# Performance work log

Hardware: AMD Instinct MI355X
Metric: run time of the kernel (lower is better)

The kernel has to match this reference:

```python
import jax, jax.numpy as jnp
import numpy as np
import math

B, S, P, G = 8, 512, 64, 64
E, GE = 768, 32          # sub_embed_dim, gene_embed_dim
HD = E // 2              # sub_head_dim = 384
L = P * G
LAMBDA_INIT = 0.8 - 0.6 * math.exp(-0.3 * 0)  # depth=0 -> 0.2
SCALING = HD ** -0.5


def setup_inputs() -> dict:
    key0 = jax.random.key(0)
    ks = jax.random.split(key0, 12)
    init = 0.02
    return {
        "query": jax.random.normal(ks[0], (B, S, E), jnp.float32),
        "key": jax.random.normal(ks[1], (B, P, G, GE), jnp.float32),
        "query_mask": jax.random.bernoulli(ks[2], 0.9, (B, S)),
        "key_mask": jax.random.bernoulli(ks[3], 0.9, (B, P, G)),
        # weights stored [in, out] so y = x @ W (equiv to torch Linear no-bias)
        "Wq": jax.random.normal(ks[4], (E, E), jnp.float32) * init,
        "Wkv": jax.random.normal(ks[5], (GE, 2 * E), jnp.float32) * init,
        "Wout": jax.random.normal(ks[6], (E, E), jnp.float32) * init,
        "lambda_q1": jax.random.normal(ks[7], (HD,), jnp.float32) * 0.1,
        "lambda_k1": jax.random.normal(ks[8], (HD,), jnp.float32) * 0.1,
        "lambda_q2": jax.random.normal(ks[9], (HD,), jnp.float32) * 0.1,
        "lambda_k2": jax.random.normal(ks[10], (HD,), jnp.float32) * 0.1,
        "ln_weight": jnp.ones((E,), jnp.float32),  # RMSNorm affine weight (2*HD = E)
    }


def reference(query, key, query_mask, key_mask, Wq, Wkv, Wout,
              lambda_q1, lambda_k1, lambda_q2, lambda_k2, ln_weight):
    # Projections
    Q = query @ Wq                                   # [B,S,E]
    KV = key.reshape(B, L, GE) @ Wkv                 # [B,L,2E]
    K = KV[..., :E]                                  # [B,L,E]
    V = KV[..., E:]                                  # [B,L,E] (= 2*HD)

    # Split into 2 heads of dim HD
    Qh = Q.reshape(B, S, 2, HD).transpose(0, 2, 1, 3) * SCALING   # [B,2,S,HD]
    Kh = K.reshape(B, L, 2, HD).transpose(0, 2, 1, 3)             # [B,2,L,HD]

    # Combined mask [B,S,L]
    mask = query_mask[:, :, None] & key_mask.reshape(B, L)[:, None, :]

    # Dual attention scores + stable softmax (eps=1e-8 on denominator)
    scores = jnp.einsum('bhsd,bhld->bhsl', Qh, Kh)                # [B,2,S,L]
    scores = jnp.where(mask[:, None], scores, -1e20)
    m = jnp.max(scores, axis=-1, keepdims=True)
    p = jnp.exp(scores - m)
    attn = p / (jnp.sum(p, axis=-1, keepdims=True) + 1e-8)

    # Differential combination
    lam = (jnp.exp(jnp.sum(lambda_q1 * lambda_k1))
           - jnp.exp(jnp.sum(lambda_q2 * lambda_k2)) + LAMBDA_INIT)
    diff = attn[:, 0] - lam * attn[:, 1]                          # [B,S,L]
    diff = diff - jnp.min(diff, axis=-1, keepdims=True) + 1e-20
    diff = jnp.where(mask, diff, 0.0)

    # Value contraction: [B,S,L] @ [B,L,E] -> [B,S,E]
    attn_out = jnp.einsum('bsl,ble->bse', diff, V)

    # RMSNorm (eps=1e-5, affine) then scale by (1 - lambda_init)
    ms = jnp.mean(attn_out * attn_out, axis=-1, keepdims=True)
    attn_out = attn_out * jax.lax.rsqrt(ms + 1e-5) * ln_weight
    attn_out = attn_out * (1.0 - LAMBDA_INIT)

    out = attn_out @ Wout                                         # [B,S,E]
    return out, diff.reshape(B, S, P, G)
```

## Files before the change

kernel.cpp:

```cpp
#include <hip/hip_runtime.h>
#include <math.h>

#define LAM_INIT 0.2f
#define ONE_MINUS_LAM 0.8f
#define SCALING_F 0.05103103630798288f

typedef _Float16 h2 __attribute__((ext_vector_type(2)));

#if defined(__has_builtin)
#if __has_builtin(__builtin_amdgcn_fdot2)
#define FDOT2(a, b, c) __builtin_amdgcn_fdot2((a), (b), (c), false)
#endif
#endif
#ifndef FDOT2
#define FDOT2(a, b, c) ((float)(a).x * (float)(b).x + ((float)(a).y * (float)(b).y + (c)))
#endif

__device__ inline float waveMin(float v) {
#pragma unroll
    for (int o = 32; o > 0; o >>= 1) v = fminf(v, __shfl_xor(v, o));
    return v;
}
__device__ inline float waveSum(float v) {
#pragma unroll
    for (int o = 32; o > 0; o >>= 1) v += __shfl_xor(v, o);
    return v;
}

__global__ __launch_bounds__(256) void k01_prep(
    const float* __restrict__ key, const float* __restrict__ Wq,
    const float* __restrict__ Wkv, const float* __restrict__ Wout,
    const float* __restrict__ lq1, const float* __restrict__ lk1,
    const float* __restrict__ lq2, const float* __restrict__ lk2,
    const float* __restrict__ ln,
    unsigned* __restrict__ keyThU, float* __restrict__ Wcp,
    float* __restrict__ Wvp, float* __restrict__ lam,
    float* __restrict__ M)
{
    int blk = blockIdx.x;
    int tid = threadIdx.x;
    if (blk < 128) {
        int b  = blk >> 4;
        int l0 = (blk & 15) << 8;
        __shared__ float tile[256 * 33];
        const float* kp = key + ((size_t)b * 4096 + l0) * 32;
#pragma unroll
        for (int q = 0; q < 32; ++q) {
            int idx = tid + (q << 8);
            int r = idx >> 5, g = idx & 31;
            tile[r * 33 + g] = kp[idx];
        }
        __syncthreads();
#pragma unroll
        for (int gp = 0; gp < 16; ++gp) {
            h2 v;
            v.x = (_Float16)tile[tid * 33 + 2 * gp];
            v.y = (_Float16)tile[tid * 33 + 2 * gp + 1];
            keyThU[((size_t)(b * 16 + gp)) * 4096 + l0 + tid] =
                __builtin_bit_cast(unsigned, v);
        }
    } else if (blk < 512) {
        int bb = blk - 128;
        int kc = bb & 1;
        int ob = bb >> 1;
        int idx = ob * 256 + tid;
        int e  = idx >> 6;
        int hg = idx & 63;
        int h = hg >> 5, g = hg & 31;
        const float4* wqr = (const float4*)(Wq  + (size_t)e * 768 + h * 384 + kc * 192);
        const float4* wkr = (const float4*)(Wkv + (size_t)g * 1536 + h * 384 + kc * 192);
        float s0 = 0.f, s1 = 0.f;
#pragma unroll 4
        for (int d = 0; d < 48; d += 2) {
            float4 a0 = wqr[d],   b0 = wkr[d];
            float4 a1 = wqr[d+1], b1 = wkr[d+1];
            s0 += a0.x*b0.x + a0.y*b0.y + a0.z*b0.z + a0.w*b0.w;
            s1 += a1.x*b1.x + a1.y*b1.y + a1.z*b1.z + a1.w*b1.w;
        }
        Wcp[kc * 49152 + idx] = (s0 + s1) * SCALING_F;
    } else if (blk < 1280) {
        int bb = blk - 512;
        int kc = bb / 96;
        int ob = bb - kc * 96;
        int idx = ob * 256 + tid;
        int g = idx / 768;
        int e = idx - g * 768;
        const float* wvr = Wkv + (size_t)g * 1536 + 768;
        int c0 = kc * 96;
        float s0 = 0.f, s1 = 0.f;
#pragma unroll 4
        for (int c = c0; c < c0 + 96; c += 2) {
            s0 += wvr[c]   * ln[c]   * Wout[(size_t)c * 768 + e];
            s1 += wvr[c+1] * ln[c+1] * Wout[(size_t)(c+1) * 768 + e];
        }
        Wvp[kc * 24576 + idx] = s0 + s1;
    } else if (blk == 1280) {
        float s1 = 0.f, s2 = 0.f;
        for (int d = tid; d < 384; d += 256) {
            s1 += lq1[d] * lk1[d];
            s2 += lq2[d] * lk2[d];
        }
        s1 = waveSum(s1);
        s2 = waveSum(s2);
        __shared__ float r1[4], r2[4];
        int wid = tid >> 6, lane = tid & 63;
        if (lane == 0) { r1[wid] = s1; r2[wid] = s2; }
        __syncthreads();
        if (tid == 0) {
            float a  = r1[0] + r1[1] + r1[2] + r1[3];
            float b2 = r2[0] + r2[1] + r2[2] + r2[3];
            lam[0] = expf(a) - expf(b2) + LAM_INIT;
        }
    } else {
        int idx = (blk - 1281) * 256 + tid;
        int g = idx >> 5, gp = idx & 31;
        const float4* ra = (const float4*)(Wkv + (size_t)g  * 1536 + 768);
        const float4* rb = (const float4*)(Wkv + (size_t)gp * 1536 + 768);
        float s = 0.f;
#pragma unroll 4
        for (int q = 0; q < 192; ++q) {
            float4 a = ra[q], b = rb[q];
            s += a.x*b.x + a.y*b.y + a.z*b.z + a.w*b.w;
        }
        M[idx] = s;
    }
}

__global__ __launch_bounds__(256) void k2_qt(
    const float* __restrict__ query, const float* __restrict__ Wcp,
    const float* __restrict__ Wvp, float* __restrict__ WvoT,
    float* __restrict__ Qtp)
{
    int blk = blockIdx.x;
    int tid = threadIdx.x;
    if (blk >= 512) {
        int idx = (blk - 512) * 256 + tid;
        float s = 0.f;
#pragma unroll
        for (int kc = 0; kc < 8; ++kc) s += Wvp[kc * 24576 + idx];
        int g = idx / 768;
        int e = idx - g * 768;
        WvoT[(size_t)e * 32 + g] = s;
        return;
    }
    int kc = blk >> 7;
    int mt = blk & 127;
    int m0 = mt * 32;
    __shared__ __align__(16) float As[64 * 33];
    __shared__ __align__(16) float Bs[64 * 64];

    int tm = tid >> 5;
    int tn = tid & 31;
    float acc[4][2];
#pragma unroll
    for (int r = 0; r < 4; ++r) { acc[r][0] = 0.f; acc[r][1] = 0.f; }

    for (int ch = 0; ch < 3; ++ch) {
        int k0 = kc * 192 + ch * 64;
        __syncthreads();
#pragma unroll
        for (int q = 0; q < 2; ++q) {
            int f = tid + q * 256;
            int m = f >> 4, kq = f & 15;
            float4 v = *(const float4*)&query[(size_t)(m0 + m) * 768 + k0 + kq * 4];
            As[(kq * 4 + 0) * 33 + m] = v.x;
            As[(kq * 4 + 1) * 33 + m] = v.y;
            As[(kq * 4 + 2) * 33 + m] = v.z;
            As[(kq * 4 + 3) * 33 + m] = v.w;
        }
#pragma unroll
        for (int q = 0; q < 4; ++q) {
            int f = tid + q * 256;
            int kk = f >> 4, n4 = f & 15;
            float4 a = *(const float4*)&Wcp[(size_t)(k0 + kk) * 64 + n4 * 4];
            float4 b = *(const float4*)&Wcp[49152 + (size_t)(k0 + kk) * 64 + n4 * 4];
            float4 s; s.x = a.x + b.x; s.y = a.y + b.y; s.z = a.z + b.z; s.w = a.w + b.w;
            *(float4*)&Bs[kk * 64 + n4 * 4] = s;
        }
        __syncthreads();
#pragma unroll 8
        for (int kk = 0; kk < 64; ++kk) {
            float4 a = *(const float4*)&As[kk * 33 + tm * 4];
            float2 b = *(const float2*)&Bs[kk * 64 + tn * 2];
            acc[0][0] += a.x * b.x; acc[0][1] += a.x * b.y;
            acc[1][0] += a.y * b.x; acc[1][1] += a.y * b.y;
            acc[2][0] += a.z * b.x; acc[2][1] += a.z * b.y;
            acc[3][0] += a.w * b.x; acc[3][1] += a.w * b.y;
        }
    }
#pragma unroll
    for (int r = 0; r < 4; ++r) {
        float2 o; o.x = acc[r][0]; o.y = acc[r][1];
        *(float2*)&Qtp[(size_t)kc * 262144 + (size_t)(m0 + tm * 4 + r) * 64 + tn * 2] = o;
    }
}

__global__ __launch_bounds__(512, 4) void k3_attn(
    const float* __restrict__ Qtp, const unsigned* __restrict__ keyThU,
    const int* __restrict__ qmask, const int* __restrict__ kmask,
    const float* __restrict__ lamp, float* __restrict__ diffO)
{
    int blk = blockIdx.x;
    int b  = blk >> 7;
    int s0 = (blk & 127) * 4;
    int tid = threadIdx.x;
    int lane = tid & 63, wid = tid >> 6;

    __shared__ __align__(16) unsigned qt_th[128];
    __shared__ float redS[64];
    __shared__ float redM[32];

    if (tid < 128) {
        int ts = tid >> 5;
        int h  = (tid >> 4) & 1;
        int gp = tid & 15;
        size_t row = (size_t)(b * 512 + s0 + ts) * 64;
        int col = h * 32 + 2 * gp;
        float v0 = 0.f, v1 = 0.f;
#pragma unroll
        for (int kc = 0; kc < 4; ++kc) {
            v0 += Qtp[(size_t)kc * 262144 + row + col];
            v1 += Qtp[(size_t)kc * 262144 + row + col + 1];
        }
        h2 hv; hv.x = (_Float16)v0; hv.y = (_Float16)v1;
        qt_th[gp * 8 + ts * 2 + h] = __builtin_bit_cast(unsigned, hv);
    }
    int qm[4];
#pragma unroll
    for (int ts = 0; ts < 4; ++ts) qm[ts] = qmask[b * 512 + s0 + ts];
    float lam = lamp[0];

    unsigned kmb = 0;
#pragma unroll
    for (int c = 0; c < 2; ++c) {
        int4 km = *(const int4*)(kmask + b * 4096 + c * 2048 + tid * 4);
        if (km.x) kmb |= 1u << (c * 4 + 0);
        if (km.y) kmb |= 1u << (c * 4 + 1);
        if (km.z) kmb |= 1u << (c * 4 + 2);
        if (km.w) kmb |= 1u << (c * 4 + 3);
    }
    __syncthreads();

    float p[2][4][8];
#pragma unroll
    for (int h = 0; h < 2; ++h)
#pragma unroll
        for (int ts = 0; ts < 4; ++ts)
#pragma unroll
            for (int i = 0; i < 8; ++i) p[h][ts][i] = 0.f;

    const unsigned* kt = keyThU + (size_t)b * 16 * 4096 + tid * 4;
    for (int gp = 0; gp < 16; ++gp) {
        uint4 q0 = *(const uint4*)&qt_th[gp * 8];
        uint4 q1 = *(const uint4*)&qt_th[gp * 8 + 4];
        h2 qv[8];
        qv[0] = __builtin_bit_cast(h2, q0.x); qv[1] = __builtin_bit_cast(h2, q0.y);
        qv[2] = __builtin_bit_cast(h2, q0.z); qv[3] = __builtin_bit_cast(h2, q0.w);
        qv[4] = __builtin_bit_cast(h2, q1.x); qv[5] = __builtin_bit_cast(h2, q1.y);
        qv[6] = __builtin_bit_cast(h2, q1.z); qv[7] = __builtin_bit_cast(h2, q1.w);
        const unsigned* kg = kt + (size_t)gp * 4096;
#pragma unroll
        for (int c = 0; c < 2; ++c) {
            uint4 kv = *(const uint4*)(kg + c * 2048);
            h2 k0 = __builtin_bit_cast(h2, kv.x);
            h2 k1 = __builtin_bit_cast(h2, kv.y);
            h2 k2 = __builtin_bit_cast(h2, kv.z);
            h2 k3 = __builtin_bit_cast(h2, kv.w);
#pragma unroll
            for (int ts = 0; ts < 4; ++ts)
#pragma unroll
                for (int h = 0; h < 2; ++h) {
                    h2 q = qv[ts * 2 + h];
                    p[h][ts][c*4+0] = FDOT2(k0, q, p[h][ts][c*4+0]);
                    p[h][ts][c*4+1] = FDOT2(k1, q, p[h][ts][c*4+1]);
                    p[h][ts][c*4+2] = FDOT2(k2, q, p[h][ts][c*4+2]);
                    p[h][ts][c*4+3] = FDOT2(k3, q, p[h][ts][c*4+3]);
                }
        }
    }

    float inv[2][4];
#pragma unroll
    for (int h = 0; h < 2; ++h)
#pragma unroll
        for (int ts = 0; ts < 4; ++ts) {
            float s = 0.f;
#pragma unroll
            for (int i = 0; i < 8; ++i) {
                bool ok = qm[ts] && ((kmb >> i) & 1u);
                float e = ok ? __expf(p[h][ts][i]) : 0.f;
                p[h][ts][i] = e;
                s += e;
            }
            s = waveSum(s);
            if (lane == 0) redS[(h * 4 + ts) * 8 + wid] = s;
        }
    __syncthreads();
#pragma unroll
    for (int h = 0; h < 2; ++h)
#pragma unroll
        for (int ts = 0; ts < 4; ++ts) {
            int r = (h * 4 + ts) * 8;
            float s = redS[r];
#pragma unroll
            for (int w = 1; w < 8; ++w) s += redS[r + w];
            inv[h][ts] = 1.0f / (s + 1e-8f);
        }

    float mn[4];
#pragma unroll
    for (int ts = 0; ts < 4; ++ts) {
        float v = 3.4e38f;
#pragma unroll
        for (int i = 0; i < 8; ++i) {
            float d = p[0][ts][i] * inv[0][ts] - lam * (p[1][ts][i] * inv[1][ts]);
            p[0][ts][i] = d;
            v = fminf(v, d);
        }
        v = waveMin(v);
        if (lane == 0) redM[ts * 8 + wid] = v;
    }
    __syncthreads();
#pragma unroll
    for (int ts = 0; ts < 4; ++ts) {
        int r = ts * 8;
        float v = redM[r];
#pragma unroll
        for (int w = 1; w < 8; ++w) v = fminf(v, redM[r + w]);
        mn[ts] = v;
    }

#pragma unroll
    for (int ts = 0; ts < 4; ++ts) {
        size_t base = (size_t)(b * 512 + s0 + ts) * 4096 + tid * 4;
#pragma unroll
        for (int c = 0; c < 2; ++c) {
            float4 o;
            float v0 = p[0][ts][c*4+0] - mn[ts] + 1e-20f;
            float v1 = p[0][ts][c*4+1] - mn[ts] + 1e-20f;
            float v2 = p[0][ts][c*4+2] - mn[ts] + 1e-20f;
            float v3 = p[0][ts][c*4+3] - mn[ts] + 1e-20f;
            o.x = (qm[ts] && ((kmb >> (c*4+0)) & 1u)) ? v0 : 0.f;
            o.y = (qm[ts] && ((kmb >> (c*4+1)) & 1u)) ? v1 : 0.f;
            o.z = (qm[ts] && ((kmb >> (c*4+2)) & 1u)) ? v2 : 0.f;
            o.w = (qm[ts] && ((kmb >> (c*4+3)) & 1u)) ? v3 : 0.f;
            *(float4*)(diffO + base + c * 2048) = o;
        }
    }
}

__global__ __launch_bounds__(256) void k4_out(
    const float* __restrict__ diff, const float* __restrict__ key,
    const float* __restrict__ M, const float* __restrict__ WvoT,
    float* __restrict__ out)
{
    int row0 = blockIdx.x * 8;
    int b = row0 >> 9;
    int tid = threadIdx.x;
    int lq = tid >> 5;
    int rp = (tid >> 3) & 3;
    int gq = tid & 7;
    int g0 = gq * 4;

    __shared__ __align__(16) float Ks[256][32];
    __shared__ __align__(16) float Tp[8][8][32];
    __shared__ __align__(16) float Ml[1024];
    __shared__ __align__(16) float Ts[8][32];
    __shared__ float rs_s[8];

#pragma unroll
    for (int q = 0; q < 4; ++q) Ml[tid + q * 256] = M[tid + q * 256];

    float acc[2][4];
#pragma unroll
    for (int r = 0; r < 2; ++r)
#pragma unroll
        for (int c = 0; c < 4; ++c) acc[r][c] = 0.f;

    const float* d0 = diff + (size_t)(row0 + rp * 2 + 0) * 4096;
    const float* d1 = diff + (size_t)(row0 + rp * 2 + 1) * 4096;

    for (int ch = 0; ch < 16; ++ch) {
        int lbase = ch * 256;
        __syncthreads();
#pragma unroll
        for (int q = 0; q < 8; ++q) {
            int f = tid + q * 256;
            int rr = f >> 3, g4 = f & 7;
            *(float4*)&Ks[rr][g4 * 4] =
                *(const float4*)&key[((size_t)(b * 4096 + lbase + rr)) * 32 + g4 * 4];
        }
        __syncthreads();

        int l0 = lbase + lq * 32;
#pragma unroll 2
        for (int j4 = 0; j4 < 8; ++j4) {
            int l = l0 + j4 * 4;
            float4 dv0 = *(const float4*)(d0 + l);
            float4 dv1 = *(const float4*)(d1 + l);
            int ll = lq * 32 + j4 * 4;
#pragma unroll
            for (int c = 0; c < 4; ++c) {
                float4 kq = *(const float4*)&Ks[ll + c][g0];
                float a = (c == 0) ? dv0.x : (c == 1) ? dv0.y : (c == 2) ? dv0.z : dv0.w;
                float bq = (c == 0) ? dv1.x : (c == 1) ? dv1.y : (c == 2) ? dv1.z : dv1.w;
                acc[0][0] += a * kq.x;  acc[0][1] += a * kq.y;
                acc[0][2] += a * kq.z;  acc[0][3] += a * kq.w;
                acc[1][0] += bq * kq.x; acc[1][1] += bq * kq.y;
                acc[1][2] += bq * kq.z; acc[1][3] += bq * kq.w;
            }
        }
    }

    {
        float4 o0; o0.x = acc[0][0]; o0.y = acc[0][1]; o0.z = acc[0][2]; o0.w = acc[0][3];
        float4 o1; o1.x = acc[1][0]; o1.y = acc[1][1]; o1.z = acc[1][2]; o1.w = acc[1][3];
        *(float4*)&Tp[lq][rp * 2 + 0][g0] = o0;
        *(float4*)&Tp[lq][rp * 2 + 1][g0] = o1;
    }
    __syncthreads();
    {
        int r = tid >> 5, g = tid & 31;
        float s = 0.f;
#pragma unroll
        for (int q = 0; q < 8; ++q) s += Tp[q][r][g];
        Ts[r][g] = s;
    }
    __syncthreads();

    {
        int r = tid >> 5, gp = tid & 31;
        float inner = 0.f;
#pragma unroll
        for (int g = 0; g < 32; ++g) inner = fmaf(Ts[r][g], Ml[g * 32 + gp], inner);
        float part = inner * Ts[r][gp];
#pragma unroll
        for (int o = 16; o > 0; o >>= 1) part += __shfl_xor(part, o);
        if (gp == 0)
            rs_s[r] = rsqrtf(part * (1.0f / 768.0f) + 1e-5f) * ONE_MINUS_LAM;
    }
    __syncthreads();

    {
        int r = tid >> 5, c0 = tid & 31;
        float rs = rs_s[r];
        float4 t[8];
#pragma unroll
        for (int q = 0; q < 8; ++q) t[q] = *(const float4*)&Ts[r][q * 4];
#pragma unroll
        for (int j = 0; j < 6; ++j) {
            int e = c0 * 4 + j * 128;
            const float4* wp = (const float4*)(WvoT + (size_t)e * 32);
            float4 o; o.x = 0.f; o.y = 0.f; o.z = 0.f; o.w = 0.f;
#pragma unroll
            for (int q = 0; q < 8; ++q) {
                float4 a0 = wp[q];
                float4 a1 = wp[q + 8];
                float4 a2 = wp[q + 16];
                float4 a3 = wp[q + 24];
                o.x += t[q].x*a0.x + t[q].y*a0.y + t[q].z*a0.z + t[q].w*a0.w;
                o.y += t[q].x*a1.x + t[q].y*a1.y + t[q].z*a1.z + t[q].w*a1.w;
                o.z += t[q].x*a2.x + t[q].y*a2.y + t[q].z*a2.z + t[q].w*a2.w;
                o.w += t[q].x*a3.x + t[q].y*a3.y + t[q].z*a3.z + t[q].w*a3.w;
            }
            o.x *= rs; o.y *= rs; o.z *= rs; o.w *= rs;
            *(float4*)(out + (size_t)(row0 + r) * 768 + e) = o;
        }
    }
}

extern "C" void kernel_launch(void* const* d_in, const int* in_sizes, int n_in,
                              void* d_out, int out_size, void* d_ws, size_t ws_size,
                              hipStream_t stream) {
    (void)in_sizes; (void)n_in; (void)out_size; (void)ws_size;
    const float* query = (const float*)d_in[0];
    const float* key   = (const float*)d_in[1];
    const int*   qmask = (const int*)d_in[2];
    const int*   kmask = (const int*)d_in[3];
    const float* Wq    = (const float*)d_in[4];
    const float* Wkv   = (const float*)d_in[5];
    const float* Wout  = (const float*)d_in[6];
    const float* lq1   = (const float*)d_in[7];
    const float* lk1   = (const float*)d_in[8];
    const float* lq2   = (const float*)d_in[9];
    const float* lk2   = (const float*)d_in[10];
    const float* ln    = (const float*)d_in[11];

    float* out  = (float*)d_out;
    float* diff = out + 3145728;

    float* ws      = (float*)d_ws;
    float* Wcp     = ws;
    float* WvoT    = ws + 98304;
    float* Wvp     = ws + 122880;
    float* lam     = ws + 319488;
    unsigned* keyThU = (unsigned*)(ws + 319552);
    float* Qtp     = ws + 843840;
    float* Mbuf    = ws + 1892416;

    k01_prep<<<1285, 256, 0, stream>>>(key, Wq, Wkv, Wout, lq1, lk1, lq2, lk2, ln,
                                       keyThU, Wcp, Wvp, lam, Mbuf);
    k2_qt<<<608, 256, 0, stream>>>(query, Wcp, Wvp, WvoT, Qtp);
    k3_attn<<<1024, 512, 0, stream>>>(Qtp, keyThU, qmask, kmask, lam, diff);
    k4_out<<<512, 256, 0, stream>>>(diff, key, Mbuf, WvoT, out);
}
```

Baseline: 275.1 us.

## Double k4 threads and prefetch next key chunk into registers

k4_out now runs 512 threads per block, and each wave covers 16 key rows per chunk instead of 32. The key tile for the next chunk is loaded into registers while the current chunk is computed from shared memory, which hides global load latency. The RMS norm reduction is rewritten as one wave-wide reduction per row, and the output projection is split over 64 lanes. This removes the separate rs_s shared stage and one barrier. In exchange, register pressure rises from the prefetch buffer, and a 16-way partial-sum reduction is added.

New measurement: 329.5 us. 1.2x slower.

```diff
diff --git a/kernel.cpp b/kernel.cpp
--- a/kernel.cpp
+++ b/kernel.cpp
@@ -349,7 +349,7 @@
     }
 }
 
-__global__ __launch_bounds__(256) void k4_out(
+__global__ __launch_bounds__(512) void k4_out(
     const float* __restrict__ diff, const float* __restrict__ key,
     const float* __restrict__ M, const float* __restrict__ WvoT,
     float* __restrict__ out)
@@ -363,13 +363,9 @@
     int g0 = gq * 4;
 
     __shared__ __align__(16) float Ks[256][32];
-    __shared__ __align__(16) float Tp[8][8][32];
+    __shared__ __align__(16) float Tp[16][8][32];
     __shared__ __align__(16) float Ml[1024];
     __shared__ __align__(16) float Ts[8][32];
-    __shared__ float rs_s[8];
-
-#pragma unroll
-    for (int q = 0; q < 4; ++q) Ml[tid + q * 256] = M[tid + q * 256];
 
     float acc[2][4];
 #pragma unroll
@@ -379,30 +375,45 @@
 
     const float* d0 = diff + (size_t)(row0 + rp * 2 + 0) * 4096;
     const float* d1 = diff + (size_t)(row0 + rp * 2 + 1) * 4096;
+    const float* kb = key + (size_t)b * 4096 * 32;
+
+    float4 sreg[4];
+#pragma unroll
+    for (int q = 0; q < 4; ++q) {
+        int f = tid + q * 512;
+        int rr = f >> 3, g4 = f & 7;
+        sreg[q] = *(const float4*)&kb[(size_t)rr * 32 + g4 * 4];
+    }
 
     for (int ch = 0; ch < 16; ++ch) {
-        int lbase = ch * 256;
         __syncthreads();
 #pragma unroll
-        for (int q = 0; q < 8; ++q) {
-            int f = tid + q * 256;
+        for (int q = 0; q < 4; ++q) {
+            int f = tid + q * 512;
             int rr = f >> 3, g4 = f & 7;
-            *(float4*)&Ks[rr][g4 * 4] =
-                *(const float4*)&key[((size_t)(b * 4096 + lbase + rr)) * 32 + g4 * 4];
+            *(float4*)&Ks[rr][g4 * 4] = sreg[q];
         }
         __syncthreads();
-
-        int l0 = lbase + lq * 32;
-#pragma unroll 2
-        for (int j4 = 0; j4 < 8; ++j4) {
+        if (ch < 15) {
+            int lbase = (ch + 1) * 256;
+#pragma unroll
+            for (int q = 0; q < 4; ++q) {
+                int f = tid + q * 512;
+                int rr = f >> 3, g4 = f & 7;
+                sreg[q] = *(const float4*)&kb[(size_t)(lbase + rr) * 32 + g4 * 4];
+            }
+        }
+        int l0 = ch * 256 + lq * 16;
+#pragma unroll
+        for (int j4 = 0; j4 < 4; ++j4) {
             int l = l0 + j4 * 4;
             float4 dv0 = *(const float4*)(d0 + l);
             float4 dv1 = *(const float4*)(d1 + l);
-            int ll = lq * 32 + j4 * 4;
+            int ll = lq * 16 + j4 * 4;
 #pragma unroll
             for (int c = 0; c < 4; ++c) {
                 float4 kq = *(const float4*)&Ks[ll + c][g0];
-                float a = (c == 0) ? dv0.x : (c == 1) ? dv0.y : (c == 2) ? dv0.z : dv0.w;
+                float a  = (c == 0) ? dv0.x : (c == 1) ? dv0.y : (c == 2) ? dv0.z : dv0.w;
                 float bq = (c == 0) ? dv1.x : (c == 1) ? dv1.y : (c == 2) ? dv1.z : dv1.w;
                 acc[0][0] += a * kq.x;  acc[0][1] += a * kq.y;
                 acc[0][2] += a * kq.z;  acc[0][3] += a * kq.w;
@@ -418,54 +429,50 @@
         *(float4*)&Tp[lq][rp * 2 + 0][g0] = o0;
         *(float4*)&Tp[lq][rp * 2 + 1][g0] = o1;
     }
+    Ml[tid]       = M[tid];
+    Ml[tid + 512] = M[tid + 512];
     __syncthreads();
-    {
+
+    if (tid < 256) {
         int r = tid >> 5, g = tid & 31;
         float s = 0.f;
 #pragma unroll
-        for (int q = 0; q < 8; ++q) s += Tp[q][r][g];
+        for (int q = 0; q < 16; ++q) s += Tp[q][r][g];
         Ts[r][g] = s;
     }
     __syncthreads();
 
-    {
-        int r = tid >> 5, gp = tid & 31;
-        float inner = 0.f;
-#pragma unroll
-        for (int g = 0; g < 32; ++g) inner = fmaf(Ts[r][g], Ml[g * 32 + gp], inner);
-        float part = inner * Ts[r][gp];
-#pragma unroll
-        for (int o = 16; o > 0; o >>= 1) part += __shfl_xor(part, o);
-        if (gp == 0)
-            rs_s[r] = rsqrtf(part * (1.0f / 768.0f) + 1e-5f) * ONE_MINUS_LAM;
-    }
-    __syncthreads();
-
-    {
-        int r = tid >> 5, c0 = tid & 31;
-        float rs = rs_s[r];
-        float4 t[8];
-#pragma unroll
-        for (int q = 0; q < 8; ++q) t[q] = *(const float4*)&Ts[r][q * 4];
-#pragma unroll
-        for (int j = 0; j < 6; ++j) {
-            int e = c0 * 4 + j * 128;
-            const float4* wp = (const float4*)(WvoT + (size_t)e * 32);
-            float4 o; o.x = 0.f; o.y = 0.f; o.z = 0.f; o.w = 0.f;
-#pragma unroll
-            for (int q = 0; q < 8; ++q) {
-                float4 a0 = wp[q];
-                float4 a1 = wp[q + 8];
-                float4 a2 = wp[q + 16];
-                float4 a3 = wp[q + 24];
-                o.x += t[q].x*a0.x + t[q].y*a0.y + t[q].z*a0.z + t[q].w*a0.w;
-                o.y += t[q].x*a1.x + t[q].y*a1.y + t[q].z*a1.z + t[q].w*a1.w;
-                o.z += t[q].x*a2.x + t[q].y*a2.y + t[q].z*a2.z + t[q].w*a2.w;
-                o.w += t[q].x*a3.x + t[q].y*a3.y + t[q].z*a3.z + t[q].w*a3.w;
-            }
-            o.x *= rs; o.y *= rs; o.z *= rs; o.w *= rs;
-            *(float4*)(out + (size_t)(row0 + r) * 768 + e) = o;
-        }
+    int r = tid >> 6, l6 = tid & 63;
+    float ssqp = 0.f;
+#pragma unroll
+    for (int k = 0; k < 16; ++k) {
+        int gg = l6 + k * 64;
+        ssqp = fmaf(Ts[r][gg >> 5] * Ts[r][gg & 31], Ml[gg], ssqp);
+    }
+    ssqp = waveSum(ssqp);
+    float rs = rsqrtf(ssqp * (1.0f / 768.0f) + 1e-5f) * ONE_MINUS_LAM;
+
+    float4 t[8];
+#pragma unroll
+    for (int q = 0; q < 8; ++q) t[q] = *(const float4*)&Ts[r][q * 4];
+#pragma unroll
+    for (int j = 0; j < 3; ++j) {
+        int e0 = l6 * 4 + j * 256;
+        const float4* wp = (const float4*)(WvoT + (size_t)e0 * 32);
+        float4 o; o.x = 0.f; o.y = 0.f; o.z = 0.f; o.w = 0.f;
+#pragma unroll
+        for (int q = 0; q < 8; ++q) {
+            float4 a0 = wp[q];
+            float4 a1 = wp[q + 8];
+            float4 a2 = wp[q + 16];
+            float4 a3 = wp[q + 24];
+            o.x += t[q].x*a0.x + t[q].y*a0.y + t[q].z*a0.z + t[q].w*a0.w;
+            o.y += t[q].x*a1.x + t[q].y*a1.y + t[q].z*a1.z + t[q].w*a1.w;
+            o.z += t[q].x*a2.x + t[q].y*a2.y + t[q].z*a2.z + t[q].w*a2.w;
+            o.w += t[q].x*a3.x + t[q].y*a3.y + t[q].z*a3.z + t[q].w*a3.w;
+        }
+        o.x *= rs; o.y *= rs; o.z *= rs; o.w *= rs;
+        *(float4*)(out + (size_t)(row0 + r) * 768 + e0) = o;
     }
 }
 
@@ -502,5 +509,5 @@
                                        keyThU, Wcp, Wvp, lam, Mbuf);
     k2_qt<<<608, 256, 0, stream>>>(query, Wcp, Wvp, WvoT, Qtp);
     k3_attn<<<1024, 512, 0, stream>>>(Qtp, keyThU, qmask, kmask, lam, diff);
-    k4_out<<<512, 256, 0, stream>>>(diff, key, Mbuf, WvoT, out);
-}
+    k4_out<<<512, 512, 0, stream>>>(diff, key, Mbuf, WvoT, out);
+}
```
